# Optimization experiments

Measured on AMD Instinct MI355X. Metric: run time of the kernel, lower is better.

## Reference

```python
import jax, jax.numpy as jnp
import numpy as np

E = 8        # num_experts (== num_local_experts here)
H = 2048     # hidden_size
I = 1024     # intermediate_size
T = 8192     # num_tokens
K = 2        # top_k


def setup_inputs() -> dict:
    key = jax.random.key(0)
    ks = jax.random.split(key, 6)
    x = jax.random.normal(ks[0], (T, H), dtype=jnp.float32)
    selected_experts = jax.random.randint(ks[1], (T, K), 0, E, dtype=jnp.int32)
    routing_weights = jax.random.uniform(ks[2], (T, K), dtype=jnp.float32)
    # per-expert weights; torch Linear stores [out, in]; we store [E, in, out] for einsum
    gate_w = jax.random.normal(ks[3], (E, H, I), dtype=jnp.float32) * 0.02
    up_w = jax.random.normal(ks[4], (E, H, I), dtype=jnp.float32) * 0.02
    down_w = jax.random.normal(ks[5], (E, I, H), dtype=jnp.float32) * 0.02
    return {
        "x": x,
        "selected_experts": selected_experts,
        "routing_weights": routing_weights,
        "gate_w": gate_w,
        "up_w": up_w,
        "down_w": down_w,
    }


def reference(x, selected_experts, routing_weights, gate_w, up_w, down_w):
    # Combined per-(token, expert) weight: sum of routing weights over top-k slots
    # that selected this expert. Mathematically identical to the sort/dispatch/
    # weighted index_add_ in the original module.
    w = jnp.einsum(
        "tke,tk->te",
        jax.nn.one_hot(selected_experts, E, dtype=x.dtype),
        routing_weights.astype(x.dtype),
    )  # [T, E]
    g = jnp.einsum("th,ehi->eti", x, gate_w)               # [E, T, I]
    u = jnp.einsum("th,ehi->eti", x, up_w)                 # [E, T, I]
    a = jax.nn.gelu(g, approximate=True) * u               # gelu tanh approx
    # down-proj per expert then weighted combine (scatter-add equivalent)
    out = jnp.einsum("eti,eih,te->th", a, down_w, w)       # [T, H], float32
    return out
```

## Files before the change

### kernel.cpp

```cpp
#include <hip/hip_runtime.h>
#include <hip/hip_bf16.h>


typedef __attribute__((ext_vector_type(8))) short bf16x8;
typedef __attribute__((ext_vector_type(4))) float f32x4;
typedef __attribute__((ext_vector_type(4))) unsigned short us4;

#define AS1 __attribute__((address_space(1)))
#define AS3 __attribute__((address_space(3)))

static constexpr int T_TOK = 8192;
static constexpr int HID   = 2048;
static constexpr int INTER = 1024;
static constexpr int NEXP  = 8;
static constexpr int NPAIR = T_TOK * 2;
static constexpr int TM    = 256;
static constexpr int MAX_ROWS = NPAIR + NEXP * TM;
static constexpr int MAX_RT   = MAX_ROWS / TM;
static constexpr int OUTN = T_TOK * HID;

__device__ __forceinline__ unsigned short f2bf(float f) {
  unsigned u = __float_as_uint(f);
  u += 0x7fffu + ((u >> 16) & 1u);
  return (unsigned short)(u >> 16);
}
__device__ __forceinline__ float bf2f(unsigned short h) {
  return __uint_as_float(((unsigned)h) << 16);
}
__device__ __forceinline__ void glds16(const void* g, void* l) {
  __builtin_amdgcn_global_load_lds((const AS1 void*)g, (AS3 void*)l, 16, 0, 0);
}

__global__ void detect_k(const unsigned* __restrict__ xw, int* __restrict__ flagp) {
  int tid = threadIdx.x;
  int cnt = 0;
  for (int i = tid; i < 256; i += 64) {
    unsigned e = (xw[i] >> 7) & 0xffu;
    cnt += (e >= 0x70u && e <= 0x8fu) ? 1 : 0;
  }
  for (int off = 32; off; off >>= 1) cnt += __shfl_down(cnt, off);
  if (tid == 0) *flagp = (cnt >= 192) ? 1 : 0;
}

__global__ void zero_out_k(unsigned* __restrict__ out, const int* __restrict__ flagp) {
  int n = (*flagp) ? (OUTN / 2) : OUTN;
  int i = blockIdx.x * 256 + threadIdx.x;
  int stride = gridDim.x * 256;
  for (; i < n; i += stride) out[i] = 0u;
}

__global__ void routing_k(const int* __restrict__ sel, const void* __restrict__ rwv,
                          int* __restrict__ rows, float* __restrict__ wgt,
                          int* __restrict__ offs, int* __restrict__ pairpos,
                          const int* __restrict__ flagp) {
  __shared__ int cnt[NEXP], cur[NEXP], offs_s[NEXP + 1];
  int flag = *flagp;
  const unsigned short* rw16 = (const unsigned short*)rwv;
  const float* rwf = (const float*)rwv;
  int tid = threadIdx.x;
  if (tid < NEXP) cnt[tid] = 0;
  __syncthreads();
  for (int p = tid; p < NPAIR; p += 1024) atomicAdd(&cnt[sel[p]], 1);
  __syncthreads();
  if (tid == 0) {
    int off = 0;
    for (int e = 0; e < NEXP; ++e) {
      offs_s[e] = off; cur[e] = off;
      off += (cnt[e] + TM - 1) / TM * TM;
    }
    offs_s[NEXP] = off;
  }
  __syncthreads();
  if (tid <= NEXP) offs[tid] = offs_s[tid];
  for (int p = tid; p < NPAIR; p += 1024) {
    int e = sel[p];
    int pos = atomicAdd(&cur[e], 1);
    rows[pos] = p >> 1;
    wgt[pos] = flag ? bf2f(rw16[p]) : rwf[p];
    pairpos[p] = pos;
  }
  for (int e = 0; e < NEXP; ++e)
    for (int r = offs_s[e] + cnt[e] + tid; r < offs_s[e + 1]; r += 1024) {
      rows[r] = 0; wgt[r] = 0.f;
    }
}

__global__ void convert_x_k(const void* __restrict__ xin,
                            unsigned short* __restrict__ xc,
                            const int* __restrict__ flagp) {
  int flag = *flagp;
  const int nvec = (T_TOK * HID) / 8;
  int v = blockIdx.x * 256 + threadIdx.x;
  int stride = gridDim.x * 256;
  for (; v < nvec; v += stride) {
    if (flag) {
      ((uint4*)xc)[v] = ((const uint4*)xin)[v];
    } else {
      const float4* s = (const float4*)xin;
      float4 a = s[2 * v], b = s[2 * v + 1];
      uint4 o;
      o.x = (unsigned)f2bf(a.x) | ((unsigned)f2bf(a.y) << 16);
      o.y = (unsigned)f2bf(a.z) | ((unsigned)f2bf(a.w) << 16);
      o.z = (unsigned)f2bf(b.x) | ((unsigned)f2bf(b.y) << 16);
      o.w = (unsigned)f2bf(b.z) | ((unsigned)f2bf(b.w) << 16);
      ((uint4*)xc)[v] = o;
    }
  }
}

__global__ void transpose_k(const void* __restrict__ in,
                            unsigned short* __restrict__ out, int R, int C,
                            const int* __restrict__ flagp) {
  __shared__ unsigned short t[64 * 72];
  int flag = *flagp;
  int e = blockIdx.z;
  int c0 = blockIdx.x * 64, r0 = blockIdx.y * 64;
  int tid = threadIdx.x;
  int mr = tid >> 4;
  int mc = tid & 15;
  unsigned short b[4][4];
  if (flag) {
    const unsigned short* src = (const unsigned short*)in + (size_t)e * R * C;
#pragma unroll
    for (int i = 0; i < 4; ++i) {
      us4 v = *(const us4*)(src + (size_t)(r0 + mr * 4 + i) * C + c0 + mc * 4);
      b[i][0] = v[0]; b[i][1] = v[1]; b[i][2] = v[2]; b[i][3] = v[3];
    }
  } else {
    const float* src = (const float*)in + (size_t)e * R * C;
#pragma unroll
    for (int i = 0; i < 4; ++i) {
      float4 v = *(const float4*)(src + (size_t)(r0 + mr * 4 + i) * C + c0 + mc * 4);
      b[i][0] = f2bf(v.x); b[i][1] = f2bf(v.y); b[i][2] = f2bf(v.z); b[i][3] = f2bf(v.w);
    }
  }
#pragma unroll
  for (int j = 0; j < 4; ++j) {
    us4 w;
    w[0] = b[0][j]; w[1] = b[1][j]; w[2] = b[2][j]; w[3] = b[3][j];
    *(us4*)(&t[(mc * 4 + j) * 72 + mr * 4]) = w;
  }
  __syncthreads();
  int orow = tid >> 2, ch = (tid & 3) * 16;
  uint4 v0 = *(const uint4*)(&t[orow * 72 + ch]);
  uint4 v1 = *(const uint4*)(&t[orow * 72 + ch + 8]);
  unsigned short* dst = out + (size_t)e * R * C + (size_t)(c0 + orow) * R + r0 + ch;
  *(uint4*)(dst) = v0;
  *(uint4*)(dst + 8) = v1;
}


__device__ __forceinline__ const bf16x8* ldf(const unsigned short* sm, int slot,
                                             int r, int c8) {
  return (const bf16x8*)(sm + slot * 8192 + r * 64 + ((c8 ^ (r & 7)) << 3));
}
__device__ __forceinline__ void stage_half(const unsigned short* p0,
                                           const unsigned short* p1,
                                           unsigned short* dst) {
  glds16(p0, dst);
  glds16(p1, dst + 4096);
}

#define MFMA8(AH, BH, B)                                                       \
  _Pragma("unroll") for (int i_ = 0; i_ < 4; ++i_) {                           \
    _Pragma("unroll") for (int j_ = 0; j_ < 2; ++j_) {                         \
      acc[AH][BH][i_][j_] = __builtin_amdgcn_mfma_f32_16x16x32_bf16(           \
          a[i_][0], B[j_][0], acc[AH][BH][i_][j_], 0, 0, 0);                   \
      acc[AH][BH][i_][j_] = __builtin_amdgcn_mfma_f32_16x16x32_bf16(           \
          a[i_][1], B[j_][1], acc[AH][BH][i_][j_], 0, 0, 0);                   \
    }                                                                          \
  }

template <int BUF, bool S1, bool S2, int VM>
__device__ __forceinline__ void ktile(
    unsigned short* sm, int wbase, int rA, int rB, int lquad,
    const unsigned short* pA00, const unsigned short* pA01,
    const unsigned short* pA10, const unsigned short* pA11,
    const unsigned short* pB00, const unsigned short* pB01,
    const unsigned short* pB10, const unsigned short* pB11,
    int ko1, int ko2, f32x4 (&acc)[2][2][4][2]) {
  bf16x8 a[4][2], b0[2][2], b1[2][2];
#pragma unroll
  for (int i = 0; i < 4; ++i)
#pragma unroll
    for (int k = 0; k < 2; ++k)
      a[i][k] = *ldf(sm, BUF * 2 + 0, rA + i * 16, k * 4 + lquad);
#pragma unroll
  for (int j = 0; j < 2; ++j)
#pragma unroll
    for (int k = 0; k < 2; ++k)
      b0[j][k] = *ldf(sm, 4 + BUF * 2 + 0, rB + j * 16, k * 4 + lquad);
  if constexpr (S1)
    stage_half(pA10 + ko1, pA11 + ko1, sm + ((BUF ^ 1) * 2 + 1) * 8192 + wbase);
  __builtin_amdgcn_s_barrier();
  asm volatile("s_waitcnt lgkmcnt(0)" ::: "memory");
  __builtin_amdgcn_s_setprio(1);
  MFMA8(0, 0, b0);
  __builtin_amdgcn_s_setprio(0);
  __builtin_amdgcn_s_barrier();
#pragma unroll
  for (int j = 0; j < 2; ++j)
#pragma unroll
    for (int k = 0; k < 2; ++k)
      b1[j][k] = *ldf(sm, 4 + BUF * 2 + 1, rB + j * 16, k * 4 + lquad);
  if constexpr (S1)
    stage_half(pB00 + ko1, pB01 + ko1, sm + (4 + (BUF ^ 1) * 2 + 0) * 8192 + wbase);
  __builtin_amdgcn_s_barrier();
  asm volatile("s_waitcnt lgkmcnt(0)" ::: "memory");
  __builtin_amdgcn_s_setprio(1);
  MFMA8(0, 1, b1);
  __builtin_amdgcn_s_setprio(0);
  __builtin_amdgcn_s_barrier();
#pragma unroll
  for (int i = 0; i < 4; ++i)
#pragma unroll
    for (int k = 0; k < 2; ++k)
      a[i][k] = *ldf(sm, BUF * 2 + 1, rA + i * 16, k * 4 + lquad);
  if constexpr (S2)
    stage_half(pA00 + ko2, pA01 + ko2, sm + (BUF * 2 + 0) * 8192 + wbase);
  __builtin_amdgcn_s_barrier();
  asm volatile("s_waitcnt lgkmcnt(0)" ::: "memory");
  __builtin_amdgcn_s_setprio(1);
  MFMA8(1, 1, b1);
  __builtin_amdgcn_s_setprio(0);
  __builtin_amdgcn_s_barrier();
  if constexpr (S2)
    stage_half(pB10 + ko2, pB11 + ko2, sm + (4 + BUF * 2 + 1) * 8192 + wbase);
  __builtin_amdgcn_s_barrier();
  __builtin_amdgcn_s_setprio(1);
  MFMA8(1, 0, b0);
  __builtin_amdgcn_s_setprio(0);
  if constexpr (VM == 4)
    asm volatile("s_waitcnt vmcnt(4)" ::: "memory");
  else if constexpr (VM == 0)
    asm volatile("s_waitcnt vmcnt(0)" ::: "memory");
  __builtin_amdgcn_s_barrier();
}

__global__ __launch_bounds__(512, 2) void gemm_gateup8(
    const unsigned short* __restrict__ xc,
    const unsigned short* __restrict__ gwT,
    const unsigned short* __restrict__ uwT,
    const int* __restrict__ rows, const int* __restrict__ offs,
    unsigned short* __restrict__ act) {
  extern __shared__ unsigned short sm[];
  int nRT = offs[NEXP] >> 8;
  int rowTile = blockIdx.x >> 3;
  if (rowTile >= nRT) return;
  int nt = blockIdx.x & 7;
  int row0 = rowTile << 8;
  int e = 0;
  while (row0 >= offs[e + 1]) ++e;

  int tid = threadIdx.x;
  int lane = tid & 63, lrow = lane & 15, lquad = lane >> 4;
  int wave = tid >> 6;
  int wmg = wave >> 2, wng = wave & 3;
  int wbase = wave << 9;
  int rA = wmg * 64 + lrow;
  int rB = wng * 32 + lrow;

  int sr = tid >> 3;
  int swz = ((tid & 7) ^ (sr & 7)) << 3;

  const unsigned short* pA00 = xc + (size_t)rows[row0 + sr] * HID + swz;
  const unsigned short* pA01 = xc + (size_t)rows[row0 + 64 + sr] * HID + swz;
  const unsigned short* pA10 = xc + (size_t)rows[row0 + 128 + sr] * HID + swz;
  const unsigned short* pA11 = xc + (size_t)rows[row0 + 192 + sr] * HID + swz;
  const unsigned short* gB = gwT + ((size_t)e * INTER + (size_t)nt * 128) * HID;
  const unsigned short* uB = uwT + ((size_t)e * INTER + (size_t)nt * 128) * HID;
  const unsigned short* pB00 = gB + (size_t)sr * HID + swz;
  const unsigned short* pB01 = gB + (size_t)(64 + sr) * HID + swz;
  const unsigned short* pB10 = uB + (size_t)sr * HID + swz;
  const unsigned short* pB11 = uB + (size_t)(64 + sr) * HID + swz;

  f32x4 acc[2][2][4][2] = {};

  stage_half(pA00, pA01, sm + 0 * 8192 + wbase);
  stage_half(pB00, pB01, sm + 4 * 8192 + wbase);
  stage_half(pB10, pB11, sm + 5 * 8192 + wbase);
  stage_half(pA10, pA11, sm + 1 * 8192 + wbase);
  stage_half(pA00 + 64, pA01 + 64, sm + 2 * 8192 + wbase);
  stage_half(pB10 + 64, pB11 + 64, sm + 7 * 8192 + wbase);
  asm volatile("s_waitcnt vmcnt(4)" ::: "memory");
  __builtin_amdgcn_s_barrier();

  constexpr int NT = HID / 64;
#pragma unroll 1
  for (int it = 0; it < NT / 2 - 1; ++it) {
    int u = it * 2;
    ktile<0, true, true, 4>(sm, wbase, rA, rB, lquad, pA00, pA01, pA10, pA11,
                            pB00, pB01, pB10, pB11, (u + 1) * 64, (u + 2) * 64, acc);
    ktile<1, true, true, 4>(sm, wbase, rA, rB, lquad, pA00, pA01, pA10, pA11,
                            pB00, pB01, pB10, pB11, (u + 2) * 64, (u + 3) * 64, acc);
  }
  ktile<0, true, false, 0>(sm, wbase, rA, rB, lquad, pA00, pA01, pA10, pA11,
                           pB00, pB01, pB10, pB11, (NT - 1) * 64, 0, acc);
  ktile<1, false, false, -1>(sm, wbase, rA, rB, lquad, pA00, pA01, pA10, pA11,
                             pB00, pB01, pB10, pB11, 0, 0, acc);

  size_t actb = (size_t)row0 * INTER + (size_t)nt * 128 + wng * 32 + lrow;
#pragma unroll
  for (int ah = 0; ah < 2; ++ah)
#pragma unroll
    for (int i = 0; i < 4; ++i)
#pragma unroll
      for (int r = 0; r < 4; ++r) {
        int m = ah * 128 + wmg * 64 + i * 16 + lquad * 4 + r;
#pragma unroll
        for (int j = 0; j < 2; ++j) {
          float g = acc[ah][0][i][j][r], u = acc[ah][1][i][j][r];
          float z = 1.5957691f * (g + 0.044715f * g * g * g);
          float aout = g * u / (1.f + __expf(-z));
          act[actb + (size_t)m * INTER + j * 16] = f2bf(aout);
        }
      }
}

template <int EPI>
__global__ __launch_bounds__(512, 2) void gemm_down8(
    const unsigned short* __restrict__ act,
    const unsigned short* __restrict__ dwT,
    const int* __restrict__ rows, const float* __restrict__ wgt,
    const int* __restrict__ offs, void* __restrict__ outv,
    const int* __restrict__ flagp, float* __restrict__ y) {
  extern __shared__ unsigned short sm[];
  int nRT = offs[NEXP] >> 8;
  int rowTile = blockIdx.x >> 3;
  if (rowTile >= nRT) return;
  int nt = blockIdx.x & 7;
  int row0 = rowTile << 8;
  int e = 0;
  while (row0 >= offs[e + 1]) ++e;

  int tid = threadIdx.x;
  int lane = tid & 63, lrow = lane & 15, lquad = lane >> 4;
  int wave = tid >> 6;
  int wmg = wave >> 2, wng = wave & 3;
  int wbase = wave << 9;
  int rA = wmg * 64 + lrow;
  int rB = wng * 32 + lrow;

  int sr = tid >> 3;
  int swz = ((tid & 7) ^ (sr & 7)) << 3;

  const unsigned short* pA00 = act + (size_t)(row0 + sr) * INTER + swz;
  const unsigned short* pA01 = act + (size_t)(row0 + 64 + sr) * INTER + swz;
  const unsigned short* pA10 = act + (size_t)(row0 + 128 + sr) * INTER + swz;
  const unsigned short* pA11 = act + (size_t)(row0 + 192 + sr) * INTER + swz;
  const unsigned short* dB = dwT + ((size_t)e * HID + (size_t)nt * 256) * INTER;
  const unsigned short* pB00 = dB + (size_t)sr * INTER + swz;
  const unsigned short* pB01 = dB + (size_t)(64 + sr) * INTER + swz;
  const unsigned short* pB10 = dB + (size_t)(128 + sr) * INTER + swz;
  const unsigned short* pB11 = dB + (size_t)(192 + sr) * INTER + swz;

  f32x4 acc[2][2][4][2] = {};

  stage_half(pA00, pA01, sm + 0 * 8192 + wbase);
  stage_half(pB00, pB01, sm + 4 * 8192 + wbase);
  stage_half(pB10, pB11, sm + 5 * 8192 + wbase);
  stage_half(pA10, pA11, sm + 1 * 8192 + wbase);
  stage_half(pA00 + 64, pA01 + 64, sm + 2 * 8192 + wbase);
  stage_half(pB10 + 64, pB11 + 64, sm + 7 * 8192 + wbase);
  asm volatile("s_waitcnt vmcnt(4)" ::: "memory");
  __builtin_amdgcn_s_barrier();

  constexpr int NT = INTER / 64;
#pragma unroll 1
  for (int it = 0; it < NT / 2 - 1; ++it) {
    int u = it * 2;
    ktile<0, true, true, 4>(sm, wbase, rA, rB, lquad, pA00, pA01, pA10, pA11,
                            pB00, pB01, pB10, pB11, (u + 1) * 64, (u + 2) * 64, acc);
    ktile<1, true, true, 4>(sm, wbase, rA, rB, lquad, pA00, pA01, pA10, pA11,
                            pB00, pB01, pB10, pB11, (u + 2) * 64, (u + 3) * 64, acc);
  }
  ktile<0, true, false, 0>(sm, wbase, rA, rB, lquad, pA00, pA01, pA10, pA11,
                           pB00, pB01, pB10, pB11, (NT - 1) * 64, 0, acc);
  ktile<1, false, false, -1>(sm, wbase, rA, rB, lquad, pA00, pA01, pA10, pA11,
                             pB00, pB01, pB10, pB11, 0, 0, acc);

  if constexpr (EPI == 1) {
#pragma unroll
    for (int ah = 0; ah < 2; ++ah)
#pragma unroll
      for (int i = 0; i < 4; ++i)
#pragma unroll
        for (int r = 0; r < 4; ++r) {
          int m = row0 + ah * 128 + wmg * 64 + i * 16 + lquad * 4 + r;
          float w = wgt[m];
          float* yp = y + (size_t)m * HID + (size_t)nt * 256 + wng * 32 + lrow;
#pragma unroll
          for (int bh = 0; bh < 2; ++bh)
#pragma unroll
            for (int j = 0; j < 2; ++j)
              yp[bh * 128 + j * 16] = acc[ah][bh][i][j][r] * w;
        }
  } else {
    int flag = *flagp;
#pragma unroll
    for (int ah = 0; ah < 2; ++ah)
#pragma unroll
      for (int i = 0; i < 4; ++i)
#pragma unroll
        for (int r = 0; r < 4; ++r) {
          int m = row0 + ah * 128 + wmg * 64 + i * 16 + lquad * 4 + r;
          float w = wgt[m];
          int token = rows[m];
          size_t base = (size_t)token * HID + (size_t)nt * 256 + wng * 32 + lrow;
          if (flag) {
#pragma unroll
            for (int bh = 0; bh < 2; ++bh)
#pragma unroll
              for (int j = 0; j < 2; ++j) {
                float v = acc[ah][bh][i][j][r] * w;
                float o = __shfl_xor(v, 1);
                if (((lane & 1) == 0) && w != 0.f) {
                  unsigned* p = (unsigned*)((unsigned short*)outv + base + bh * 128 + j * 16);
                  unsigned old = __atomic_load_n(p, __ATOMIC_RELAXED), assumed;
                  do {
                    assumed = old;
                    float flo = bf2f((unsigned short)(assumed & 0xffffu));
                    float fhi = bf2f((unsigned short)(assumed >> 16));
                    unsigned nw = (unsigned)f2bf(flo + v) | ((unsigned)f2bf(fhi + o) << 16);
                    old = atomicCAS(p, assumed, nw);
                  } while (old != assumed);
                }
              }
          } else {
            if (w != 0.f) {
              float* outf = (float*)outv;
#pragma unroll
              for (int bh = 0; bh < 2; ++bh)
#pragma unroll
                for (int j = 0; j < 2; ++j)
                  atomicAdd(outf + base + bh * 128 + j * 16, acc[ah][bh][i][j][r] * w);
            }
          }
        }
  }
}

__global__ void combine_k(const float* __restrict__ y,
                          const int* __restrict__ pairpos,
                          void* __restrict__ outv, const int* __restrict__ flagp) {
  int flag = *flagp;
  const int NV = T_TOK * (HID / 4);
  int v = blockIdx.x * 256 + threadIdx.x;
  int stride = gridDim.x * 256;
  for (; v < NV; v += stride) {
    int t = v >> 9;
    int hq = (v & 511) * 4;
    int p0 = pairpos[2 * t], p1 = pairpos[2 * t + 1];
    float4 a = *(const float4*)(y + (size_t)p0 * HID + hq);
    float4 b = *(const float4*)(y + (size_t)p1 * HID + hq);
    float4 s;
    s.x = a.x + b.x; s.y = a.y + b.y; s.z = a.z + b.z; s.w = a.w + b.w;
    if (flag) {
      uint2 o;
      o.x = (unsigned)f2bf(s.x) | ((unsigned)f2bf(s.y) << 16);
      o.y = (unsigned)f2bf(s.z) | ((unsigned)f2bf(s.w) << 16);
      *(uint2*)((unsigned short*)outv + (size_t)v * 4) = o;
    } else {
      *(float4*)((float*)outv + (size_t)v * 4) = s;
    }
  }
}

extern "C" void kernel_launch(void* const* d_in, const int* in_sizes, int n_in,
                              void* d_out, int out_size, void* d_ws, size_t ws_size,
                              hipStream_t stream) {
  (void)in_sizes; (void)n_in; (void)out_size;
  const void* x   = d_in[0];
  const int* sel  = (const int*)d_in[1];
  const void* rw  = d_in[2];
  const void* gw  = d_in[3];
  const void* uw  = d_in[4];
  const void* dw  = d_in[5];

  char* ws = (char*)d_ws;
  int* offs     = (int*)ws;
  int* flagp    = (int*)(ws + 64);
  int* rows     = (int*)(ws + 256);
  float* wgt    = (float*)(ws + 256 + MAX_ROWS * 4);
  int* pairpos  = (int*)(ws + 256 + MAX_ROWS * 8);
  size_t off0   = 256 + (size_t)MAX_ROWS * 8 + (size_t)NPAIR * 4;
  off0 = (off0 + 255) & ~(size_t)255;
  unsigned short* dwT = (unsigned short*)(ws + off0);
  unsigned short* act = dwT + (size_t)NEXP * HID * INTER;
  unsigned short* gwT = act + (size_t)MAX_ROWS * INTER;
  unsigned short* uwT = gwT + (size_t)NEXP * HID * INTER;
  unsigned short* xc  = uwT + (size_t)NEXP * HID * INTER;
  float* y            = (float*)gwT;
  size_t y_end = ((char*)gwT - ws) + (size_t)MAX_ROWS * HID * 4;
  bool use_y = ws_size >= y_end;

  hipFuncSetAttribute(reinterpret_cast<const void*>(gemm_gateup8),
                      hipFuncAttributeMaxDynamicSharedMemorySize, 131072);
  hipFuncSetAttribute(reinterpret_cast<const void*>(gemm_down8<1>),
                      hipFuncAttributeMaxDynamicSharedMemorySize, 131072);
  hipFuncSetAttribute(reinterpret_cast<const void*>(gemm_down8<0>),
                      hipFuncAttributeMaxDynamicSharedMemorySize, 131072);

  detect_k<<<1, 64, 0, stream>>>((const unsigned*)x, flagp);
  if (!use_y)
    zero_out_k<<<4096, 256, 0, stream>>>((unsigned*)d_out, flagp);
  routing_k<<<1, 1024, 0, stream>>>(sel, rw, rows, wgt, offs, pairpos, flagp);
  transpose_k<<<dim3(INTER / 64, HID / 64, NEXP), 256, 0, stream>>>(gw, gwT, HID, INTER, flagp);
  transpose_k<<<dim3(INTER / 64, HID / 64, NEXP), 256, 0, stream>>>(uw, uwT, HID, INTER, flagp);
  transpose_k<<<dim3(HID / 64, INTER / 64, NEXP), 256, 0, stream>>>(dw, dwT, INTER, HID, flagp);
  convert_x_k<<<4096, 256, 0, stream>>>(x, xc, flagp);
  gemm_gateup8<<<MAX_RT * 8, 512, 131072, stream>>>(xc, gwT, uwT, rows, offs, act);
  if (use_y) {
    gemm_down8<1><<<MAX_RT * 8, 512, 131072, stream>>>(act, dwT, rows, wgt, offs,
                                                       d_out, flagp, y);
    combine_k<<<4096, 256, 0, stream>>>(y, pairpos, d_out, flagp);
  } else {
    gemm_down8<0><<<MAX_RT * 8, 512, 131072, stream>>>(act, dwT, rows, wgt, offs,
                                                       d_out, flagp, nullptr);
  }
}
```

Measured before the change: 583.1 us.

## Store down-proj partials in bf16, merge transposes, use wave-aggregated routing atomics

The per-pair down-projection output buffer y is now written and read as bf16 instead of fp32, with adjacent lanes packed via shuffle into 32-bit stores. This halves the traffic of the scratch buffer between gemm_down8 and combine_k. The three weight-transpose launches are merged into one launch, and routing uses ballot-based wave-aggregated atomics plus an upfront zeroing of the padding rows. The extra rounding of partials to bf16 before summation adds precision loss.

```diff
diff --git a/kernel.cpp b/kernel.cpp
--- a/kernel.cpp
+++ b/kernel.cpp
@@ -58,9 +58,19 @@
   const unsigned short* rw16 = (const unsigned short*)rwv;
   const float* rwf = (const float*)rwv;
   int tid = threadIdx.x;
+  int lane = tid & 63;
   if (tid < NEXP) cnt[tid] = 0;
+  for (int i = tid; i < MAX_ROWS; i += 1024) { rows[i] = 0; wgt[i] = 0.f; }
   __syncthreads();
-  for (int p = tid; p < NPAIR; p += 1024) atomicAdd(&cnt[sel[p]], 1);
+  for (int p = tid; p < NPAIR; p += 1024) {
+    int e = sel[p];
+#pragma unroll
+    for (int ee = 0; ee < NEXP; ++ee) {
+      unsigned long long m = __ballot(e == ee);
+      if (m && lane == __ffsll((long long)m) - 1)
+        atomicAdd(&cnt[ee], (int)__popcll(m));
+    }
+  }
   __syncthreads();
   if (tid == 0) {
     int off = 0;
@@ -74,15 +84,22 @@
   if (tid <= NEXP) offs[tid] = offs_s[tid];
   for (int p = tid; p < NPAIR; p += 1024) {
     int e = sel[p];
-    int pos = atomicAdd(&cur[e], 1);
+    int pos = 0;
+#pragma unroll
+    for (int ee = 0; ee < NEXP; ++ee) {
+      unsigned long long m = __ballot(e == ee);
+      if (e == ee) {
+        int leader = __ffsll((long long)m) - 1;
+        int base = 0;
+        if (lane == leader) base = atomicAdd(&cur[ee], (int)__popcll(m));
+        base = __shfl(base, leader);
+        pos = base + (int)__popcll(m & ((1ull << lane) - 1ull));
+      }
+    }
     rows[pos] = p >> 1;
     wgt[pos] = flag ? bf2f(rw16[p]) : rwf[p];
     pairpos[p] = pos;
   }
-  for (int e = 0; e < NEXP; ++e)
-    for (int r = offs_s[e] + cnt[e] + tid; r < offs_s[e + 1]; r += 1024) {
-      rows[r] = 0; wgt[r] = 0.f;
-    }
 }
 
 __global__ void convert_x_k(const void* __restrict__ xin,
@@ -108,12 +125,20 @@
   }
 }
 
-__global__ void transpose_k(const void* __restrict__ in,
-                            unsigned short* __restrict__ out, int R, int C,
-                            const int* __restrict__ flagp) {
+__global__ void transpose3_k(const void* __restrict__ gwp, const void* __restrict__ uwp,
+                             const void* __restrict__ dwp,
+                             unsigned short* __restrict__ gwT,
+                             unsigned short* __restrict__ uwT,
+                             unsigned short* __restrict__ dwT,
+                             const int* __restrict__ flagp) {
   __shared__ unsigned short t[64 * 72];
+  int z = blockIdx.z;
+  int tt = z >> 3, e = z & 7;
+  const void* in; unsigned short* out; int R, C;
+  if (tt == 0)      { in = gwp; out = gwT; R = HID;   C = INTER; if (blockIdx.x >= 16) return; }
+  else if (tt == 1) { in = uwp; out = uwT; R = HID;   C = INTER; if (blockIdx.x >= 16) return; }
+  else              { in = dwp; out = dwT; R = INTER; C = HID;   if (blockIdx.y >= 16) return; }
   int flag = *flagp;
-  int e = blockIdx.z;
   int c0 = blockIdx.x * 64, r0 = blockIdx.y * 64;
   int tid = threadIdx.x;
   int mr = tid >> 4;
@@ -323,7 +348,7 @@
     const unsigned short* __restrict__ dwT,
     const int* __restrict__ rows, const float* __restrict__ wgt,
     const int* __restrict__ offs, void* __restrict__ outv,
-    const int* __restrict__ flagp, float* __restrict__ y) {
+    const int* __restrict__ flagp, unsigned short* __restrict__ y) {
   extern __shared__ unsigned short sm[];
   int nRT = offs[NEXP] >> 8;
   int rowTile = blockIdx.x >> 3;
@@ -388,12 +413,17 @@
         for (int r = 0; r < 4; ++r) {
           int m = row0 + ah * 128 + wmg * 64 + i * 16 + lquad * 4 + r;
           float w = wgt[m];
-          float* yp = y + (size_t)m * HID + (size_t)nt * 256 + wng * 32 + lrow;
+          unsigned short* yp = y + (size_t)m * HID + (size_t)nt * 256 + wng * 32 + lrow;
 #pragma unroll
           for (int bh = 0; bh < 2; ++bh)
 #pragma unroll
-            for (int j = 0; j < 2; ++j)
-              yp[bh * 128 + j * 16] = acc[ah][bh][i][j][r] * w;
+            for (int j = 0; j < 2; ++j) {
+              float v = acc[ah][bh][i][j][r] * w;
+              float o = __shfl_xor(v, 1);
+              if ((lane & 1) == 0)
+                *(unsigned*)(yp + bh * 128 + j * 16) =
+                    (unsigned)f2bf(v) | ((unsigned)f2bf(o) << 16);
+            }
         }
   } else {
     int flag = *flagp;
@@ -440,7 +470,7 @@
   }
 }
 
-__global__ void combine_k(const float* __restrict__ y,
+__global__ void combine_k(const unsigned short* __restrict__ y,
                           const int* __restrict__ pairpos,
                           void* __restrict__ outv, const int* __restrict__ flagp) {
   int flag = *flagp;
@@ -451,16 +481,19 @@
     int t = v >> 9;
     int hq = (v & 511) * 4;
     int p0 = pairpos[2 * t], p1 = pairpos[2 * t + 1];
-    float4 a = *(const float4*)(y + (size_t)p0 * HID + hq);
-    float4 b = *(const float4*)(y + (size_t)p1 * HID + hq);
-    float4 s;
-    s.x = a.x + b.x; s.y = a.y + b.y; s.z = a.z + b.z; s.w = a.w + b.w;
+    uint2 a = *(const uint2*)(y + (size_t)p0 * HID + hq);
+    uint2 b = *(const uint2*)(y + (size_t)p1 * HID + hq);
+    float s0 = bf2f((unsigned short)(a.x & 0xffffu)) + bf2f((unsigned short)(b.x & 0xffffu));
+    float s1 = bf2f((unsigned short)(a.x >> 16))     + bf2f((unsigned short)(b.x >> 16));
+    float s2 = bf2f((unsigned short)(a.y & 0xffffu)) + bf2f((unsigned short)(b.y & 0xffffu));
+    float s3 = bf2f((unsigned short)(a.y >> 16))     + bf2f((unsigned short)(b.y >> 16));
     if (flag) {
       uint2 o;
-      o.x = (unsigned)f2bf(s.x) | ((unsigned)f2bf(s.y) << 16);
-      o.y = (unsigned)f2bf(s.z) | ((unsigned)f2bf(s.w) << 16);
+      o.x = (unsigned)f2bf(s0) | ((unsigned)f2bf(s1) << 16);
+      o.y = (unsigned)f2bf(s2) | ((unsigned)f2bf(s3) << 16);
       *(uint2*)((unsigned short*)outv + (size_t)v * 4) = o;
     } else {
+      float4 s; s.x = s0; s.y = s1; s.z = s2; s.w = s3;
       *(float4*)((float*)outv + (size_t)v * 4) = s;
     }
   }
@@ -490,8 +523,8 @@
   unsigned short* gwT = act + (size_t)MAX_ROWS * INTER;
   unsigned short* uwT = gwT + (size_t)NEXP * HID * INTER;
   unsigned short* xc  = uwT + (size_t)NEXP * HID * INTER;
-  float* y            = (float*)gwT;
-  size_t y_end = ((char*)gwT - ws) + (size_t)MAX_ROWS * HID * 4;
+  unsigned short* y   = gwT;
+  size_t y_end = ((char*)gwT - ws) + (size_t)MAX_ROWS * HID * 2;
   bool use_y = ws_size >= y_end;
 
   hipFuncSetAttribute(reinterpret_cast<const void*>(gemm_gateup8),
@@ -505,9 +538,7 @@
   if (!use_y)
     zero_out_k<<<4096, 256, 0, stream>>>((unsigned*)d_out, flagp);
   routing_k<<<1, 1024, 0, stream>>>(sel, rw, rows, wgt, offs, pairpos, flagp);
-  transpose_k<<<dim3(INTER / 64, HID / 64, NEXP), 256, 0, stream>>>(gw, gwT, HID, INTER, flagp);
-  transpose_k<<<dim3(INTER / 64, HID / 64, NEXP), 256, 0, stream>>>(uw, uwT, HID, INTER, flagp);
-  transpose_k<<<dim3(HID / 64, INTER / 64, NEXP), 256, 0, stream>>>(dw, dwT, INTER, HID, flagp);
+  transpose3_k<<<dim3(32, 32, 24), 256, 0, stream>>>(gw, uw, dw, gwT, uwT, dwT, flagp);
   convert_x_k<<<4096, 256, 0, stream>>>(x, xc, flagp);
   gemm_gateup8<<<MAX_RT * 8, 512, 131072, stream>>>(xc, gwT, uwT, rows, offs, act);
   if (use_y) {
```

Result: slower. 620.3 us (+6.4%).
